# Kernel optimization log

Hardware: AMD Instinct MI355X
Metric: run time of the kernel (lower is better)

Reference implementation:

```python
import jax, jax.numpy as jnp
import numpy as np

B, S, D = 4, 2048, 1024


def setup_inputs() -> dict:
    key = jax.random.key(0)
    ks = jax.random.split(key, 8)
    x = jax.random.normal(ks[0], (B, S, D), dtype=jnp.float32)
    # additive causal mask: 0 on/below diagonal, -1e9 above
    causal = jnp.tril(jnp.ones((S, S), dtype=bool))
    mask = jnp.where(causal, 0.0, -1e9).astype(jnp.float32)[None, :, :]  # [1,S,S]
    scale = 1.0 / np.sqrt(D)
    Wq = jax.random.normal(ks[1], (D, D), dtype=jnp.float32) * scale
    bq = jnp.zeros((D,), dtype=jnp.float32)
    Wk = jax.random.normal(ks[2], (D, D), dtype=jnp.float32) * scale
    bk = jnp.zeros((D,), dtype=jnp.float32)
    Wv = jax.random.normal(ks[3], (D, D), dtype=jnp.float32) * scale
    bv = jnp.zeros((D,), dtype=jnp.float32)
    return {"x": x, "mask": mask, "Wq": Wq, "bq": bq, "Wk": Wk, "bk": bk, "Wv": Wv, "bv": bv}


def reference(x, mask, Wq, bq, Wk, bk, Wv, bv):
    # Q/K/V projections (torch Linear: y = x @ W^T + b)
    q = jnp.einsum('bsd,ed->bse', x, Wq) + bq
    k = jnp.einsum('bsd,ed->bse', x, Wk) + bk
    v = jnp.einsum('bsd,ed->bse', x, Wv) + bv
    d = x.shape[-1]
    scores = jnp.einsum('bqd,bkd->bqk', q, k) / jnp.sqrt(jnp.float32(d))
    scores = scores + mask
    attn = jax.nn.softmax(scores, axis=-1)
    return jnp.einsum('bqk,bkd->bqd', attn, v)
```

## Files before the change

kernel.cpp:

```cpp
#include <hip/hip_runtime.h>
#include <hip/hip_bf16.h>


typedef __attribute__((ext_vector_type(8))) short short8;
typedef __attribute__((ext_vector_type(4))) float f32x4;
typedef __attribute__((ext_vector_type(4))) unsigned short ushort4v;

static __device__ __forceinline__ unsigned short f2b(float f) {
  union { __hip_bfloat16 h; unsigned short u; } cv;
  cv.h = __float2bfloat16(f);
  return cv.u;
}

__global__ __launch_bounds__(256) void cvt4(const float* __restrict__ in,
                                            unsigned short* __restrict__ out, int n4) {
  int i = blockIdx.x * blockDim.x + threadIdx.x;
  if (i >= n4) return;
  float4 v = reinterpret_cast<const float4*>(in)[i];
  ushort4v o;
  o.x = f2b(v.x); o.y = f2b(v.y); o.z = f2b(v.z); o.w = f2b(v.w);
  reinterpret_cast<ushort4v*>(out)[i] = o;
}

__global__ __launch_bounds__(256) void concat_bias(const float* __restrict__ a,
                                                   const float* __restrict__ b,
                                                   const float* __restrict__ c,
                                                   float* __restrict__ out) {
  int i = blockIdx.x * blockDim.x + threadIdx.x;
  float v = (i < 1024) ? a[i] : (i < 2048) ? b[i - 1024] : c[i - 2048];
  out[i] = v;
}

template <int MODE>
__global__ __launch_bounds__(256) void gemm128(
    const unsigned short* __restrict__ A, const unsigned short* __restrict__ B,
    void* __restrict__ Cout, const float* __restrict__ bias, float scale,
    int lda, int ldb, int ldc, int ktiles,
    long aStride, long bStride, long cStride) {
  int bx = blockIdx.x, by = blockIdx.y, bz = blockIdx.z;
  if (MODE == 1 && bx > by) return;
  int nkt = (MODE == 2) ? (by + 1) * 2 : ktiles;

  __shared__ unsigned short sA[128 * 64];
  __shared__ unsigned short sB[128 * 64];

  int tid = threadIdx.x;
  int lane = tid & 63;
  int w = tid >> 6;
  int wr = w >> 1, wc = w & 1;

  const unsigned short* Ab = A + bz * aStride + (long)by * 128 * lda;
  const unsigned short* Bb = B + bz * bStride + (long)bx * 128 * ldb;

  f32x4 acc[4][4];
#pragma unroll
  for (int m = 0; m < 4; ++m)
#pragma unroll
    for (int n = 0; n < 4; ++n) acc[m][n] = (f32x4){0.f, 0.f, 0.f, 0.f};

  for (int kt = 0; kt < nkt; ++kt) {
    __syncthreads();
#pragma unroll
    for (int c = 0; c < 8; ++c) {
      int chunk = w * 8 + c;
      int half = chunk & 15;
      int L = half * 1024 + lane * 16;
      int row = L >> 7;
      int gl = (L >> 4) & 7;
      int gs = gl ^ (row & 7);
      if (chunk < 16) {
        const unsigned short* src = Ab + (long)row * lda + kt * 64 + gs * 8;
        __builtin_amdgcn_global_load_lds(
            (const __attribute__((address_space(1))) void*)src,
            (__attribute__((address_space(3))) void*)(sA + half * 512), 16, 0, 0);
      } else {
        const unsigned short* src = Bb + (long)row * ldb + kt * 64 + gs * 8;
        __builtin_amdgcn_global_load_lds(
            (const __attribute__((address_space(1))) void*)src,
            (__attribute__((address_space(3))) void*)(sB + half * 512), 16, 0, 0);
      }
    }
    __syncthreads();

#pragma unroll
    for (int kk = 0; kk < 2; ++kk) {
      short8 af[4], bfr[4];
#pragma unroll
      for (int m = 0; m < 4; ++m) {
        int row = wr * 64 + m * 16 + (lane & 15);
        int g = kk * 4 + (lane >> 4);
        af[m] = *(const short8*)((const char*)sA + row * 128 + ((g ^ (row & 7)) << 4));
      }
#pragma unroll
      for (int n = 0; n < 4; ++n) {
        int row = wc * 64 + n * 16 + (lane & 15);
        int g = kk * 4 + (lane >> 4);
        bfr[n] = *(const short8*)((const char*)sB + row * 128 + ((g ^ (row & 7)) << 4));
      }
#pragma unroll
      for (int m = 0; m < 4; ++m)
#pragma unroll
        for (int n = 0; n < 4; ++n)
          acc[m][n] = __builtin_amdgcn_mfma_f32_16x16x32_bf16(af[m], bfr[n], acc[m][n], 0, 0, 0);
    }
  }

  int r0 = by * 128 + wr * 64 + (lane >> 4) * 4;
  int c0 = bx * 128 + wc * 64 + (lane & 15);
  if (MODE == 0) {
    unsigned short* C = (unsigned short*)Cout + bz * cStride;
#pragma unroll
    for (int m = 0; m < 4; ++m)
#pragma unroll
      for (int n = 0; n < 4; ++n) {
        int gc = c0 + n * 16;
        float bv = bias[gc];
#pragma unroll
        for (int r = 0; r < 4; ++r)
          C[(long)(r0 + m * 16 + r) * ldc + gc] = f2b(acc[m][n][r] + bv);
      }
  } else {
    float* C = (float*)Cout + bz * cStride;
#pragma unroll
    for (int m = 0; m < 4; ++m)
#pragma unroll
      for (int n = 0; n < 4; ++n)
#pragma unroll
        for (int r = 0; r < 4; ++r)
          C[(long)(r0 + m * 16 + r) * ldc + c0 + n * 16] = acc[m][n][r] * scale;
  }
}

__global__ __launch_bounds__(256) void transpose64(const unsigned short* __restrict__ V,
                                                   unsigned short* __restrict__ Vt) {
  __shared__ unsigned short t[64][72];
  int s0 = blockIdx.x * 64, d0 = blockIdx.y * 64;
  long bz = blockIdx.z;
  const unsigned short* src = V + bz * (2048L * 3072);
  unsigned short* dst = Vt + bz * (1024L * 2048);
  int tid = threadIdx.x;
#pragma unroll
  for (int pp = 0; pp < 2; ++pp) {
    int r = pp * 32 + (tid >> 3);
    int c = (tid & 7) * 8;
    short8 v = *(const short8*)(src + (long)(s0 + r) * 3072 + d0 + c);
    *(short8*)&t[r][c] = v;
  }
  __syncthreads();
#pragma unroll
  for (int pp = 0; pp < 2; ++pp) {
    int d = pp * 32 + (tid >> 3);
    int sc = (tid & 7) * 8;
    short8 v;
#pragma unroll
    for (int k = 0; k < 8; ++k) v[k] = (short)t[sc + k][d];
    *(short8*)(dst + (long)(d0 + d) * 2048 + s0 + sc) = v;
  }
}

__global__ __launch_bounds__(256) void softmax_causal(float* __restrict__ S) {
  int row = blockIdx.x;
  long b = row >> 11;
  int i = row & 2047;
  float* s = S + (b * 2048 + i) * 2048;
  unsigned short* p = (unsigned short*)s;
  int n = i + 1;
  int jEnd = ((i >> 7) + 1) << 7;
  int tid = threadIdx.x;
  __shared__ float red[4];

  float m = -3.0e38f;
  for (int j = tid; j < n; j += 256) m = fmaxf(m, s[j]);
#pragma unroll
  for (int off = 32; off > 0; off >>= 1) m = fmaxf(m, __shfl_xor(m, off));
  if ((tid & 63) == 0) red[tid >> 6] = m;
  __syncthreads();
  m = fmaxf(fmaxf(red[0], red[1]), fmaxf(red[2], red[3]));
  __syncthreads();

  float vals[8];
  float sum = 0.f;
#pragma unroll
  for (int k = 0; k < 8; ++k) {
    int j = tid + k * 256;
    float e = (j < n) ? __expf(s[j] - m) : 0.f;
    vals[k] = e;
    sum += e;
  }
#pragma unroll
  for (int off = 32; off > 0; off >>= 1) sum += __shfl_xor(sum, off);
  if ((tid & 63) == 0) red[tid >> 6] = sum;
  __syncthreads();
  sum = red[0] + red[1] + red[2] + red[3];
  float inv = 1.0f / sum;

#pragma unroll
  for (int k = 0; k < 8; ++k) {
    int j = tid + k * 256;
    if (j < jEnd) p[j] = f2b(vals[k] * inv);
  }
}

extern "C" void kernel_launch(void* const* d_in, const int* in_sizes, int n_in,
                              void* d_out, int out_size, void* d_ws, size_t ws_size,
                              hipStream_t stream) {
  const float* x = (const float*)d_in[0];
  const float* Wq = (const float*)d_in[2];
  const float* bq = (const float*)d_in[3];
  const float* Wk = (const float*)d_in[4];
  const float* bk = (const float*)d_in[5];
  const float* Wv = (const float*)d_in[6];
  const float* bv = (const float*)d_in[7];
  float* out = (float*)d_out;

  char* ws = (char*)d_ws;
  const long MB = 1 << 20;
  unsigned short* xb = (unsigned short*)(ws);
  unsigned short* Wb = (unsigned short*)(ws + 16 * MB);
  float* biasb = (float*)(ws + 22 * MB);
  unsigned short* QKV = (unsigned short*)(ws + 23 * MB);
  unsigned short* Vt = (unsigned short*)(ws + 71 * MB);
  float* Sbuf = (float*)(ws + 87 * MB);

  cvt4<<<8192, 256, 0, stream>>>(x, xb, 2097152);
  cvt4<<<1024, 256, 0, stream>>>(Wq, Wb, 262144);
  cvt4<<<1024, 256, 0, stream>>>(Wk, Wb + 1048576, 262144);
  cvt4<<<1024, 256, 0, stream>>>(Wv, Wb + 2097152, 262144);
  concat_bias<<<12, 256, 0, stream>>>(bq, bk, bv, biasb);

  gemm128<0><<<dim3(24, 64, 1), 256, 0, stream>>>(
      xb, Wb, QKV, biasb, 1.0f, 1024, 1024, 3072, 16, 0, 0, 0);

  transpose64<<<dim3(32, 16, 4), 256, 0, stream>>>(QKV + 2048, Vt);

  gemm128<1><<<dim3(16, 16, 4), 256, 0, stream>>>(
      QKV, QKV + 1024, Sbuf, nullptr, 0.03125f, 3072, 3072, 2048, 16,
      2048L * 3072, 2048L * 3072, 2048L * 2048);

  softmax_causal<<<8192, 256, 0, stream>>>(Sbuf);

  gemm128<2><<<dim3(8, 16, 4), 256, 0, stream>>>(
      (unsigned short*)Sbuf, Vt, out, nullptr, 1.0f, 4096, 2048, 1024, 0,
      2048L * 4096, 1024L * 2048, 2048L * 1024);
}
```

Baseline: 289.6 us.

## Fuse V transpose into QKV GEMM, balance causal PV GEMM, merge prep kernels

The QKV projection epilogue now writes V directly in transposed layout, which removes the separate transpose kernel and its round trip through memory. The Q/K buffer shrinks to row stride 2048. The PV GEMM becomes a dedicated 512-thread kernel in which each block handles a long and a short causal row strip, pairing strip 15-y with strip y to even out work under the causal triangle. The weight conversions and bias concat are merged into one launch, softmax caches the loaded scores in registers instead of reading them twice, and gemm128 gains a launch-bounds occupancy hint. The risks are more register pressure and strided 8-byte stores for the transposed V.

```diff
diff --git a/kernel.cpp b/kernel.cpp
--- a/kernel.cpp
+++ b/kernel.cpp
@@ -11,6 +11,11 @@
   cv.h = __float2bfloat16(f);
   return cv.u;
 }
+
+#define GLOAD_LDS16(gsrc, ldst)                                              \
+  __builtin_amdgcn_global_load_lds(                                          \
+      (const __attribute__((address_space(1))) void*)(gsrc),                 \
+      (__attribute__((address_space(3))) void*)(ldst), 16, 0, 0)
 
 __global__ __launch_bounds__(256) void cvt4(const float* __restrict__ in,
                                             unsigned short* __restrict__ out, int n4) {
@@ -22,24 +27,38 @@
   reinterpret_cast<ushort4v*>(out)[i] = o;
 }
 
-__global__ __launch_bounds__(256) void concat_bias(const float* __restrict__ a,
-                                                   const float* __restrict__ b,
-                                                   const float* __restrict__ c,
-                                                   float* __restrict__ out) {
-  int i = blockIdx.x * blockDim.x + threadIdx.x;
-  float v = (i < 1024) ? a[i] : (i < 2048) ? b[i - 1024] : c[i - 2048];
-  out[i] = v;
+__global__ __launch_bounds__(256) void prep_w(
+    const float* __restrict__ Wq, const float* __restrict__ Wk, const float* __restrict__ Wv,
+    const float* __restrict__ bq, const float* __restrict__ bk, const float* __restrict__ bv,
+    unsigned short* __restrict__ Wb, float* __restrict__ biasb) {
+  int id = blockIdx.x;
+  if (id < 3072) {
+    int sel = id >> 10;
+    const float* src = sel == 0 ? Wq : sel == 1 ? Wk : Wv;
+    int i = (id & 1023) * 256 + threadIdx.x;
+    float4 v = reinterpret_cast<const float4*>(src)[i];
+    ushort4v o;
+    o.x = f2b(v.x); o.y = f2b(v.y); o.z = f2b(v.z); o.w = f2b(v.w);
+    reinterpret_cast<ushort4v*>(Wb + (long)sel * 1048576)[i] = o;
+  } else {
+    int i = (id - 3072) * 256 + threadIdx.x;
+    if (i < 3072) {
+      int sel = i >> 10;
+      const float* src = sel == 0 ? bq : sel == 1 ? bk : bv;
+      biasb[i] = src[i & 1023];
+    }
+  }
 }
 
 template <int MODE>
-__global__ __launch_bounds__(256) void gemm128(
+__global__ __launch_bounds__(256, 4) void gemm128(
     const unsigned short* __restrict__ A, const unsigned short* __restrict__ B,
-    void* __restrict__ Cout, const float* __restrict__ bias, float scale,
+    void* __restrict__ Cout, const float* __restrict__ bias,
+    unsigned short* __restrict__ VtOut, float scale,
     int lda, int ldb, int ldc, int ktiles,
     long aStride, long bStride, long cStride) {
   int bx = blockIdx.x, by = blockIdx.y, bz = blockIdx.z;
   if (MODE == 1 && bx > by) return;
-  int nkt = (MODE == 2) ? (by + 1) * 2 : ktiles;
 
   __shared__ unsigned short sA[128 * 64];
   __shared__ unsigned short sB[128 * 64];
@@ -58,7 +77,7 @@
 #pragma unroll
     for (int n = 0; n < 4; ++n) acc[m][n] = (f32x4){0.f, 0.f, 0.f, 0.f};
 
-  for (int kt = 0; kt < nkt; ++kt) {
+  for (int kt = 0; kt < ktiles; ++kt) {
     __syncthreads();
 #pragma unroll
     for (int c = 0; c < 8; ++c) {
@@ -66,18 +85,11 @@
       int half = chunk & 15;
       int L = half * 1024 + lane * 16;
       int row = L >> 7;
-      int gl = (L >> 4) & 7;
-      int gs = gl ^ (row & 7);
+      int gs = ((L >> 4) & 7) ^ (row & 7);
       if (chunk < 16) {
-        const unsigned short* src = Ab + (long)row * lda + kt * 64 + gs * 8;
-        __builtin_amdgcn_global_load_lds(
-            (const __attribute__((address_space(1))) void*)src,
-            (__attribute__((address_space(3))) void*)(sA + half * 512), 16, 0, 0);
+        GLOAD_LDS16(Ab + (long)row * lda + kt * 64 + gs * 8, sA + half * 512);
       } else {
-        const unsigned short* src = Bb + (long)row * ldb + kt * 64 + gs * 8;
-        __builtin_amdgcn_global_load_lds(
-            (const __attribute__((address_space(1))) void*)src,
-            (__attribute__((address_space(3))) void*)(sB + half * 512), 16, 0, 0);
+        GLOAD_LDS16(Bb + (long)row * ldb + kt * 64 + gs * 8, sB + half * 512);
       }
     }
     __syncthreads();
@@ -108,17 +120,37 @@
   int r0 = by * 128 + wr * 64 + (lane >> 4) * 4;
   int c0 = bx * 128 + wc * 64 + (lane & 15);
   if (MODE == 0) {
-    unsigned short* C = (unsigned short*)Cout + bz * cStride;
-#pragma unroll
-    for (int m = 0; m < 4; ++m)
-#pragma unroll
-      for (int n = 0; n < 4; ++n) {
-        int gc = c0 + n * 16;
-        float bv = bias[gc];
-#pragma unroll
-        for (int r = 0; r < 4; ++r)
-          C[(long)(r0 + m * 16 + r) * ldc + gc] = f2b(acc[m][n][r] + bv);
-      }
+    if (bx < 16) {
+      unsigned short* C = (unsigned short*)Cout;
+#pragma unroll
+      for (int m = 0; m < 4; ++m)
+#pragma unroll
+        for (int n = 0; n < 4; ++n) {
+          int gc = c0 + n * 16;
+          float bv = bias[gc];
+#pragma unroll
+          for (int r = 0; r < 4; ++r)
+            C[(long)(r0 + m * 16 + r) * ldc + gc] = f2b(acc[m][n][r] + bv);
+        }
+    } else {
+      long b = by >> 4;
+      int s0 = (by & 15) * 128 + wr * 64 + (lane >> 4) * 4;
+      int d0 = (bx - 16) * 128 + wc * 64 + (lane & 15);
+      unsigned short* VT = VtOut + b * (1024L * 2048);
+#pragma unroll
+      for (int m = 0; m < 4; ++m)
+#pragma unroll
+        for (int n = 0; n < 4; ++n) {
+          int d = d0 + n * 16;
+          float bv = bias[2048 + d];
+          ushort4v o;
+          o.x = f2b(acc[m][n][0] + bv);
+          o.y = f2b(acc[m][n][1] + bv);
+          o.z = f2b(acc[m][n][2] + bv);
+          o.w = f2b(acc[m][n][3] + bv);
+          *(ushort4v*)(VT + (long)d * 2048 + s0 + m * 16) = o;
+        }
+    }
   } else {
     float* C = (float*)Cout + bz * cStride;
 #pragma unroll
@@ -131,30 +163,81 @@
   }
 }
 
-__global__ __launch_bounds__(256) void transpose64(const unsigned short* __restrict__ V,
-                                                   unsigned short* __restrict__ Vt) {
-  __shared__ unsigned short t[64][72];
-  int s0 = blockIdx.x * 64, d0 = blockIdx.y * 64;
-  long bz = blockIdx.z;
-  const unsigned short* src = V + bz * (2048L * 3072);
-  unsigned short* dst = Vt + bz * (1024L * 2048);
+__global__ __launch_bounds__(512, 2) void pv_gemm(
+    const unsigned short* __restrict__ P, const unsigned short* __restrict__ Vt,
+    float* __restrict__ out) {
+  __shared__ unsigned short sA[128 * 64];
+  __shared__ unsigned short sB[128 * 64];
   int tid = threadIdx.x;
-#pragma unroll
-  for (int pp = 0; pp < 2; ++pp) {
-    int r = pp * 32 + (tid >> 3);
-    int c = (tid & 7) * 8;
-    short8 v = *(const short8*)(src + (long)(s0 + r) * 3072 + d0 + c);
-    *(short8*)&t[r][c] = v;
-  }
-  __syncthreads();
-#pragma unroll
-  for (int pp = 0; pp < 2; ++pp) {
-    int d = pp * 32 + (tid >> 3);
-    int sc = (tid & 7) * 8;
-    short8 v;
-#pragma unroll
-    for (int k = 0; k < 8; ++k) v[k] = (short)t[sc + k][d];
-    *(short8*)(dst + (long)(d0 + d) * 2048 + s0 + sc) = v;
+  int lane = tid & 63;
+  int w = tid >> 6;
+  int wr = w >> 2, wc = w & 3;
+  int bx = blockIdx.x, byp = blockIdx.y, bz = blockIdx.z;
+  const unsigned short* Pb = P + bz * (2048L * 4096);
+  const unsigned short* Bb = Vt + bz * (1024L * 2048) + (long)bx * 128 * 2048;
+  float* Ob = out + bz * (2048L * 1024);
+
+#pragma unroll
+  for (int half = 0; half < 2; ++half) {
+    int strip = half == 0 ? (15 - byp) : byp;
+    int nkt = (strip + 1) * 2;
+    const unsigned short* Ab = Pb + (long)strip * 128 * 4096;
+
+    f32x4 acc[4][2];
+#pragma unroll
+    for (int m = 0; m < 4; ++m)
+#pragma unroll
+      for (int n = 0; n < 2; ++n) acc[m][n] = (f32x4){0.f, 0.f, 0.f, 0.f};
+
+    for (int kt = 0; kt < nkt; ++kt) {
+      __syncthreads();
+#pragma unroll
+      for (int c = 0; c < 4; ++c) {
+        int chunk = w * 4 + c;
+        int hh = chunk & 15;
+        int L = hh * 1024 + lane * 16;
+        int row = L >> 7;
+        int gs = ((L >> 4) & 7) ^ (row & 7);
+        if (chunk < 16) {
+          GLOAD_LDS16(Ab + (long)row * 4096 + kt * 64 + gs * 8, sA + hh * 512);
+        } else {
+          GLOAD_LDS16(Bb + (long)row * 2048 + kt * 64 + gs * 8, sB + hh * 512);
+        }
+      }
+      __syncthreads();
+
+#pragma unroll
+      for (int kk = 0; kk < 2; ++kk) {
+        short8 af[4], bf2[2];
+#pragma unroll
+        for (int m = 0; m < 4; ++m) {
+          int row = wr * 64 + m * 16 + (lane & 15);
+          int g = kk * 4 + (lane >> 4);
+          af[m] = *(const short8*)((const char*)sA + row * 128 + ((g ^ (row & 7)) << 4));
+        }
+#pragma unroll
+        for (int n = 0; n < 2; ++n) {
+          int row = wc * 32 + n * 16 + (lane & 15);
+          int g = kk * 4 + (lane >> 4);
+          bf2[n] = *(const short8*)((const char*)sB + row * 128 + ((g ^ (row & 7)) << 4));
+        }
+#pragma unroll
+        for (int m = 0; m < 4; ++m)
+#pragma unroll
+          for (int n = 0; n < 2; ++n)
+            acc[m][n] = __builtin_amdgcn_mfma_f32_16x16x32_bf16(af[m], bf2[n], acc[m][n], 0, 0, 0);
+      }
+    }
+
+    int r0 = strip * 128 + wr * 64 + (lane >> 4) * 4;
+    int c0 = bx * 128 + wc * 32 + (lane & 15);
+#pragma unroll
+    for (int m = 0; m < 4; ++m)
+#pragma unroll
+      for (int n = 0; n < 2; ++n)
+#pragma unroll
+        for (int r = 0; r < 4; ++r)
+          Ob[(long)(r0 + m * 16 + r) * 1024 + c0 + n * 16] = acc[m][n][r];
   }
 }
 
@@ -169,8 +252,14 @@
   int tid = threadIdx.x;
   __shared__ float red[4];
 
+  float vals[8];
   float m = -3.0e38f;
-  for (int j = tid; j < n; j += 256) m = fmaxf(m, s[j]);
+#pragma unroll
+  for (int k = 0; k < 8; ++k) {
+    int j = tid + k * 256;
+    vals[k] = (j < n) ? s[j] : -3.0e38f;
+    m = fmaxf(m, vals[k]);
+  }
 #pragma unroll
   for (int off = 32; off > 0; off >>= 1) m = fmaxf(m, __shfl_xor(m, off));
   if ((tid & 63) == 0) red[tid >> 6] = m;
@@ -178,12 +267,11 @@
   m = fmaxf(fmaxf(red[0], red[1]), fmaxf(red[2], red[3]));
   __syncthreads();
 
-  float vals[8];
   float sum = 0.f;
 #pragma unroll
   for (int k = 0; k < 8; ++k) {
     int j = tid + k * 256;
-    float e = (j < n) ? __expf(s[j] - m) : 0.f;
+    float e = (j < n) ? __expf(vals[k] - m) : 0.f;
     vals[k] = e;
     sum += e;
   }
@@ -218,28 +306,21 @@
   unsigned short* xb = (unsigned short*)(ws);
   unsigned short* Wb = (unsigned short*)(ws + 16 * MB);
   float* biasb = (float*)(ws + 22 * MB);
-  unsigned short* QKV = (unsigned short*)(ws + 23 * MB);
-  unsigned short* Vt = (unsigned short*)(ws + 71 * MB);
-  float* Sbuf = (float*)(ws + 87 * MB);
+  unsigned short* QK = (unsigned short*)(ws + 23 * MB);
+  unsigned short* Vt = (unsigned short*)(ws + 55 * MB);
+  float* Sbuf = (float*)(ws + 71 * MB);
 
   cvt4<<<8192, 256, 0, stream>>>(x, xb, 2097152);
-  cvt4<<<1024, 256, 0, stream>>>(Wq, Wb, 262144);
-  cvt4<<<1024, 256, 0, stream>>>(Wk, Wb + 1048576, 262144);
-  cvt4<<<1024, 256, 0, stream>>>(Wv, Wb + 2097152, 262144);
-  concat_bias<<<12, 256, 0, stream>>>(bq, bk, bv, biasb);
+  prep_w<<<3084, 256, 0, stream>>>(Wq, Wk, Wv, bq, bk, bv, Wb, biasb);
 
   gemm128<0><<<dim3(24, 64, 1), 256, 0, stream>>>(
-      xb, Wb, QKV, biasb, 1.0f, 1024, 1024, 3072, 16, 0, 0, 0);
-
-  transpose64<<<dim3(32, 16, 4), 256, 0, stream>>>(QKV + 2048, Vt);
+      xb, Wb, QK, biasb, Vt, 1.0f, 1024, 1024, 2048, 16, 0, 0, 0);
 
   gemm128<1><<<dim3(16, 16, 4), 256, 0, stream>>>(
-      QKV, QKV + 1024, Sbuf, nullptr, 0.03125f, 3072, 3072, 2048, 16,
-      2048L * 3072, 2048L * 3072, 2048L * 2048);
+      QK, QK + 1024, Sbuf, nullptr, nullptr, 0.03125f, 2048, 2048, 2048, 16,
+      2048L * 2048, 2048L * 2048, 2048L * 2048);
 
   softmax_causal<<<8192, 256, 0, stream>>>(Sbuf);
 
-  gemm128<2><<<dim3(8, 16, 4), 256, 0, stream>>>(
-      (unsigned short*)Sbuf, Vt, out, nullptr, 1.0f, 4096, 2048, 1024, 0,
-      2048L * 4096, 1024L * 2048, 2048L * 1024);
-}
+  pv_gemm<<<dim3(8, 8, 4), 512, 0, stream>>>((unsigned short*)Sbuf, Vt, out);
+}
```

Measured after the change: 301.5 us. 4.1% more time.
